# Optimization experiments

Measured on AMD Instinct MI355X. Metric: run time of the kernel, lower is better.

## Reference

```python
import jax, jax.numpy as jnp
import numpy as np
import math

B, T, C, H = 8, 512, 768, 12
ADJ_F = 12  # adj feature dim (adj_proj1 in_features)


def setup_inputs() -> dict:
    key = jax.random.key(0)
    ks = jax.random.split(key, 16)
    s = 0.02
    x = jax.random.normal(ks[0], (B, T, C), jnp.float32)
    # 1.0 marks a padded position; keep first token valid in every row
    pad = (jax.random.uniform(ks[1], (B, T)) > 0.8).astype(jnp.float32)
    pad = pad.at[:, 0].set(0.0)
    adj = jax.random.normal(ks[2], (B, T, T, ADJ_F), jnp.float32)
    # torch Linear convention: W is [out, in]
    Wq = jax.random.normal(ks[3], (C, C), jnp.float32) * s
    bq = jnp.zeros((C,), jnp.float32)
    Wk = jax.random.normal(ks[4], (C, C), jnp.float32) * s
    bk = jnp.zeros((C,), jnp.float32)
    Wv = jax.random.normal(ks[5], (C, C), jnp.float32) * s
    bv = jnp.zeros((C,), jnp.float32)
    Wp = jax.random.normal(ks[6], (C, C), jnp.float32) * s
    bp = jnp.zeros((C,), jnp.float32)
    A1 = jax.random.normal(ks[7], (2 * H, ADJ_F), jnp.float32) * s  # adj_proj1, no bias
    A2 = jax.random.normal(ks[8], (H, 2 * H), jnp.float32) * s     # adj_proj2, no bias
    adj_weight = jnp.float32(50.0)
    return dict(x=x, x_padding_judge=pad, adj=adj, Wq=Wq, bq=bq, Wk=Wk, bk=bk,
                Wv=Wv, bv=bv, Wp=Wp, bp=bp, A1=A1, A2=A2, adj_weight=adj_weight)


def reference(x, x_padding_judge, adj, Wq, bq, Wk, bk, Wv, bv, Wp, bp, A1, A2, adj_weight):
    Bx, Tx, Cx = x.shape
    hd = Cx // H
    # pairwise validity mask: [B,T,T]
    keep = 1.0 - x_padding_judge
    mask = keep[:, :, None] * keep[:, None, :]
    split = lambda h: h.reshape(Bx, Tx, H, hd).transpose(0, 2, 1, 3)  # [B,H,T,hd]
    q = split(x @ Wq.T + bq)
    k = split(x @ Wk.T + bk)
    v = split(x @ Wv.T + bv)
    att = jnp.einsum('bhqd,bhkd->bhqk', q, k) * (1.0 / math.sqrt(hd))
    # eval mode: attn_drop is identity, so the dropout-of-ones trick leaves mask unchanged
    att = jnp.where(mask[:, None, :, :] == 0.0, jnp.float32(-1e9), att)
    att = jax.nn.softmax(att, axis=-1)
    # adjacency-derived bias added AFTER softmax
    att_fix = jax.nn.gelu(jnp.einsum('bqkf,ef->bqke', adj, A1), approximate=False)
    att_fix = jnp.einsum('bqke,he->bqkh', att_fix, A2).transpose(0, 3, 1, 2)  # [B,H,T,T]
    att = att + adj_weight * att_fix
    y = jnp.einsum('bhqk,bhkd->bhqd', att, v)
    y = y.transpose(0, 2, 1, 3).reshape(Bx, Tx, Cx)
    return y @ Wp.T + bp  # resid_drop is identity in eval
```

## Files before the change

kernel.cpp:

```cpp
#include <hip/hip_runtime.h>
#include <math.h>

#define TT 512
#define CC 768
#define NH 12
#define HD 64
#define ADJF 12

typedef __attribute__((ext_vector_type(8))) short bf16x8;
typedef __attribute__((ext_vector_type(4))) float f32x4;

__device__ __forceinline__ ushort f2bf(float x) {
    unsigned u = __float_as_uint(x);
    return (ushort)((u + 0x7FFF + ((u >> 16) & 1)) >> 16);
}

#define MFMA16(a, b, c) __builtin_amdgcn_mfma_f32_16x16x32_bf16((a), (b), (c), 0, 0, 0)

__global__ __launch_bounds__(256)
void cast5(const float* __restrict__ x,  const float* __restrict__ wq,
           const float* __restrict__ wk, const float* __restrict__ wv,
           const float* __restrict__ wp,
           ushort* __restrict__ xb,  ushort* __restrict__ wqb,
           ushort* __restrict__ wkb, ushort* __restrict__ wvb,
           ushort* __restrict__ wpb)
{
    const float* src; ushort* dst; int n8;
    switch (blockIdx.y) {
      case 0:  src = x;  dst = xb;  n8 = 393216; break;
      case 1:  src = wq; dst = wqb; n8 = 73728;  break;
      case 2:  src = wk; dst = wkb; n8 = 73728;  break;
      case 3:  src = wv; dst = wvb; n8 = 73728;  break;
      default: src = wp; dst = wpb; n8 = 73728;  break;
    }
    int i = blockIdx.x * 256 + threadIdx.x;
    if (i >= n8) return;
    float4 a = ((const float4*)src)[2 * i];
    float4 b = ((const float4*)src)[2 * i + 1];
    uint4 o;
    o.x = f2bf(a.x) | ((unsigned)f2bf(a.y) << 16);
    o.y = f2bf(a.z) | ((unsigned)f2bf(a.w) << 16);
    o.z = f2bf(b.x) | ((unsigned)f2bf(b.y) << 16);
    o.w = f2bf(b.z) | ((unsigned)f2bf(b.w) << 16);
    ((uint4*)dst)[i] = o;
}

__device__ __forceinline__ void mfma_gemm_acc(
    const ushort* __restrict__ A, const ushort* __restrict__ B,
    f32x4 (&acc)[4][4], ushort* As, ushort* Bs)
{
    const int t = threadIdx.x;
    const int bm = blockIdx.x, bn = blockIdx.y;
    const int w = t >> 6, lane = t & 63, lx = lane & 15, quad = lane >> 4;
    const int wr = w >> 1, wc = w & 1;
    const int sr = t >> 1, sh = (t & 1) << 4;

    const ushort* Arow = A + (size_t)(bm * 128 + sr) * CC + sh;
    const ushort* Brow = B + (size_t)(bn * 128 + sr) * CC + sh;

    uint4 a0 = *(const uint4*)(Arow);
    uint4 a1 = *(const uint4*)(Arow + 8);
    uint4 b0 = *(const uint4*)(Brow);
    uint4 b1 = *(const uint4*)(Brow + 8);
    *(uint4*)&As[sr * 40 + sh]     = a0;
    *(uint4*)&As[sr * 40 + sh + 8] = a1;
    *(uint4*)&Bs[sr * 40 + sh]     = b0;
    *(uint4*)&Bs[sr * 40 + sh + 8] = b1;

    for (int kb = 0; kb < 24; kb++) {
        __syncthreads();
        const int cur = (kb & 1) * 5120, nxt = ((kb + 1) & 1) * 5120;
        if (kb < 23) {
            a0 = *(const uint4*)(Arow + (kb + 1) * 32);
            a1 = *(const uint4*)(Arow + (kb + 1) * 32 + 8);
            b0 = *(const uint4*)(Brow + (kb + 1) * 32);
            b1 = *(const uint4*)(Brow + (kb + 1) * 32 + 8);
        }
        bf16x8 af[4], bfr[4];
#pragma unroll
        for (int mt = 0; mt < 4; mt++)
            af[mt] = *(const bf16x8*)&As[cur + (wr * 64 + mt * 16 + lx) * 40 + quad * 8];
#pragma unroll
        for (int nt = 0; nt < 4; nt++)
            bfr[nt] = *(const bf16x8*)&Bs[cur + (wc * 64 + nt * 16 + lx) * 40 + quad * 8];
#pragma unroll
        for (int mt = 0; mt < 4; mt++)
#pragma unroll
            for (int nt = 0; nt < 4; nt++)
                acc[mt][nt] = MFMA16(af[mt], bfr[nt], acc[mt][nt]);
        if (kb < 23) {
            *(uint4*)&As[nxt + sr * 40 + sh]     = a0;
            *(uint4*)&As[nxt + sr * 40 + sh + 8] = a1;
            *(uint4*)&Bs[nxt + sr * 40 + sh]     = b0;
            *(uint4*)&Bs[nxt + sr * 40 + sh + 8] = b1;
        }
    }
}

__global__ __launch_bounds__(256)
void qkv_mfma(const ushort* __restrict__ xb,
              const ushort* __restrict__ Wqb, const float* __restrict__ bq,
              const ushort* __restrict__ Wkb, const float* __restrict__ bk,
              const ushort* __restrict__ Wvb, const float* __restrict__ bv,
              ushort* __restrict__ Qb, ushort* __restrict__ Kb,
              ushort* __restrict__ VtB)
{
    __shared__ ushort As[10240], Bs[10240];
    const int z = blockIdx.z;
    const ushort* W   = (z == 0) ? Wqb : (z == 1) ? Wkb : Wvb;
    const float* bias = (z == 0) ? bq  : (z == 1) ? bk  : bv;

    f32x4 acc[4][4];
#pragma unroll
    for (int i = 0; i < 4; i++)
#pragma unroll
        for (int j = 0; j < 4; j++) acc[i][j] = (f32x4){0.f, 0.f, 0.f, 0.f};

    mfma_gemm_acc(xb, W, acc, As, Bs);

    const int t = threadIdx.x;
    const int w = t >> 6, lane = t & 63, lx = lane & 15, quad = lane >> 4;
    const int wr = w >> 1, wc = w & 1;
    const int bm = blockIdx.x, bn = blockIdx.y;

    float bvv[4];
#pragma unroll
    for (int nt = 0; nt < 4; nt++)
        bvv[nt] = bias[bn * 128 + wc * 64 + nt * 16 + lx];

    if (z < 2) {
        ushort* O = (z == 0) ? Qb : Kb;
#pragma unroll
        for (int mt = 0; mt < 4; mt++) {
            int m0 = bm * 128 + wr * 64 + mt * 16 + quad * 4;
#pragma unroll
            for (int nt = 0; nt < 4; nt++) {
                int n = bn * 128 + wc * 64 + nt * 16 + lx;
#pragma unroll
                for (int i = 0; i < 4; i++)
                    O[(size_t)(m0 + i) * CC + n] = f2bf(acc[mt][nt][i] + bvv[nt]);
            }
        }
    } else {
#pragma unroll
        for (int mt = 0; mt < 4; mt++) {
            int m0 = bm * 128 + wr * 64 + mt * 16 + quad * 4;
            int bb = m0 >> 9, k = m0 & 511;
#pragma unroll
            for (int nt = 0; nt < 4; nt++) {
                int n = bn * 128 + wc * 64 + nt * 16 + lx;
                int hh = n >> 6, d = n & 63;
                ushort4 pk;
                pk.x = f2bf(acc[mt][nt][0] + bvv[nt]);
                pk.y = f2bf(acc[mt][nt][1] + bvv[nt]);
                pk.z = f2bf(acc[mt][nt][2] + bvv[nt]);
                pk.w = f2bf(acc[mt][nt][3] + bvv[nt]);
                *(ushort4*)&VtB[(size_t)((bb * NH + hh) * HD + d) * TT + k] = pk;
            }
        }
    }
}

__global__ __launch_bounds__(256)
void proj_mfma(const ushort* __restrict__ y1, const ushort* __restrict__ Wpb,
               const float* __restrict__ bp, float* __restrict__ out)
{
    __shared__ ushort As[10240], Bs[10240];
    f32x4 acc[4][4];
#pragma unroll
    for (int i = 0; i < 4; i++)
#pragma unroll
        for (int j = 0; j < 4; j++) acc[i][j] = (f32x4){0.f, 0.f, 0.f, 0.f};

    mfma_gemm_acc(y1, Wpb, acc, As, Bs);

    const int t = threadIdx.x;
    const int w = t >> 6, lane = t & 63, lx = lane & 15, quad = lane >> 4;
    const int wr = w >> 1, wc = w & 1;
    const int bm = blockIdx.x, bn = blockIdx.y;
#pragma unroll
    for (int nt = 0; nt < 4; nt++) {
        int n = bn * 128 + wc * 64 + nt * 16 + lx;
        float bvv = bp[n];
#pragma unroll
        for (int mt = 0; mt < 4; mt++) {
            int m0 = bm * 128 + wr * 64 + mt * 16 + quad * 4;
#pragma unroll
            for (int i = 0; i < 4; i++)
                out[(size_t)(m0 + i) * CC + n] = acc[mt][nt][i] + bvv;
        }
    }
}

__global__ __launch_bounds__(256)
void adj_f(const float* __restrict__ adj, const float* __restrict__ A1,
           const float* __restrict__ A2, const float* __restrict__ adjw_p,
           ushort* __restrict__ Fb)
{
    __shared__ float A1s[288];
    __shared__ float A2s[288];
    const int t = threadIdx.x;
    for (int i = t; i < 288; i += 256) { A1s[i] = A1[i]; A2s[i] = A2[i]; }
    __syncthreads();

    const float adjw = adjw_p[0];
    const int k = blockIdx.x * 256 + t;
    const int q = blockIdx.y;
    const int b = blockIdx.z;

    float af[12];
    size_t base = (((size_t)b * TT + q) * TT + k) * ADJF;
    *(float4*)&af[0] = *(const float4*)&adj[base + 0];
    *(float4*)&af[4] = *(const float4*)&adj[base + 4];
    *(float4*)&af[8] = *(const float4*)&adj[base + 8];

    float G[24];
#pragma unroll
    for (int e = 0; e < 24; e++) {
        float a2 = 0.f;
#pragma unroll
        for (int f = 0; f < 12; f++) a2 += A1s[e * 12 + f] * af[f];
        float z  = a2 * 0.70710678118654752f;
        float z2 = z * z;
        float er = z * (1.1283791670955126f + z2 * (-0.37612638903183754f +
                   z2 * (0.11283791670955126f + z2 * (-0.02686617064513125f +
                   z2 * (0.00522397762544218f + z2 * (-0.00085483270234508f))))));
        if (__builtin_expect(fabsf(a2) > 1.0f, 0)) er = erff(z);
        G[e] = 0.5f * a2 * (1.0f + er);
    }
#pragma unroll
    for (int hh = 0; hh < 12; hh++) {
        float a2 = 0.f;
#pragma unroll
        for (int e = 0; e < 24; e++) a2 += A2s[hh * 24 + e] * G[e];
        Fb[((size_t)(b * NH + hh) * TT + q) * TT + k] = f2bf(adjw * a2);
    }
}

__global__ __launch_bounds__(256)
void flash_mfma(const ushort* __restrict__ Qb, const ushort* __restrict__ Kb,
                const ushort* __restrict__ VtB, const ushort* __restrict__ Fb,
                const float* __restrict__ pad, ushort* __restrict__ y1)
{
    __shared__ ushort Ps[4][16][72];

    const int t = threadIdx.x, w = t >> 6, lane = t & 63;
    const int lx = lane & 15, quad = lane >> 4;
    const int qt = blockIdx.x, h = blockIdx.y, b = blockIdx.z;
    const int q0 = qt * 64;
    const int bh = b * NH + h;

    const ushort* Qrow = Qb + (size_t)(b * TT + q0 + w * 16 + lx) * CC + h * HD + quad * 8;
    bf16x8 qa0 = *(const bf16x8*)Qrow;
    bf16x8 qa1 = *(const bf16x8*)(Qrow + 32);

    const float kq = 1.0f - pad[b * TT + q0 + w * 16 + lx];

    f32x4 o[4], o2[4];
#pragma unroll
    for (int i = 0; i < 4; i++) {
        o[i]  = (f32x4){0.f, 0.f, 0.f, 0.f};
        o2[i] = (f32x4){0.f, 0.f, 0.f, 0.f};
    }
    float ls = 0.f;

    const ushort* Frow = Fb + (size_t)(bh * TT + q0 + w * 16 + lx) * TT + quad * 8;
    const float*  padk = pad + b * TT;
    const ushort* Vbase = VtB + (size_t)bh * HD * TT;

    for (int ck = 0; ck < 8; ck++) {
        const int k0 = ck * 64;
        f32x4 st[4];
        float4 kp[4];
#pragma unroll
        for (int mt = 0; mt < 4; mt++) {
            const ushort* Krow = Kb + (size_t)(b * TT + k0 + mt * 16 + lx) * CC + h * HD + quad * 8;
            bf16x8 ka0 = *(const bf16x8*)Krow;
            bf16x8 ka1 = *(const bf16x8*)(Krow + 32);
            f32x4 z = (f32x4){0.f, 0.f, 0.f, 0.f};
            z = MFMA16(ka0, qa0, z);
            z = MFMA16(ka1, qa1, z);
            st[mt] = z;
            kp[mt] = *(const float4*)&padk[k0 + mt * 16 + quad * 4];
        }
#pragma unroll
        for (int mt = 0; mt < 4; mt++) {
            float pv[4];
#pragma unroll
            for (int i = 0; i < 4; i++) {
                float kpad = ((const float*)&kp[mt])[i];
                float p = __builtin_amdgcn_exp2f(st[mt][i] * 0.18033688011112042f);
                p = (kpad != 0.0f) ? 0.0f : p;
                p = (kq == 0.0f) ? 1.0f : p;
                pv[i] = p; ls += p;
            }
            ushort4 pk;
            pk.x = f2bf(pv[0]); pk.y = f2bf(pv[1]);
            pk.z = f2bf(pv[2]); pk.w = f2bf(pv[3]);
            *(ushort4*)&Ps[w][lx][mt * 16 + quad * 4] = pk;
        }
        asm volatile("s_waitcnt lgkmcnt(0)" ::: "memory");
        bf16x8 pa0 = *(const bf16x8*)&Ps[w][lx][quad * 8];
        bf16x8 pa1 = *(const bf16x8*)&Ps[w][lx][32 + quad * 8];
        bf16x8 fa0 = *(const bf16x8*)(Frow + k0);
        bf16x8 fa1 = *(const bf16x8*)(Frow + k0 + 32);
#pragma unroll
        for (int nt = 0; nt < 4; nt++) {
            const ushort* Vrow = Vbase + (size_t)(nt * 16 + lx) * TT + k0 + quad * 8;
            bf16x8 vb0 = *(const bf16x8*)Vrow;
            bf16x8 vb1 = *(const bf16x8*)(Vrow + 32);
            o[nt]  = MFMA16(pa0, vb0, o[nt]);
            o[nt]  = MFMA16(pa1, vb1, o[nt]);
            o2[nt] = MFMA16(fa0, vb0, o2[nt]);
            o2[nt] = MFMA16(fa1, vb1, o2[nt]);
        }
    }
    ls += __shfl_xor(ls, 16, 64);
    ls += __shfl_xor(ls, 32, 64);
    float inv[4];
#pragma unroll
    for (int i = 0; i < 4; i++)
        inv[i] = 1.0f / __shfl(ls, quad * 4 + i, 16);
#pragma unroll
    for (int nt = 0; nt < 4; nt++)
#pragma unroll
        for (int i = 0; i < 4; i++)
            y1[(size_t)(b * TT + q0 + w * 16 + quad * 4 + i) * CC + h * HD + nt * 16 + lx] =
                f2bf(o[nt][i] * inv[i] + o2[nt][i]);
}

extern "C" void kernel_launch(void* const* d_in, const int* in_sizes, int n_in,
                              void* d_out, int out_size, void* d_ws, size_t ws_size,
                              hipStream_t stream)
{
    const float* x    = (const float*)d_in[0];
    const float* pad  = (const float*)d_in[1];
    const float* adj  = (const float*)d_in[2];
    const float* Wq   = (const float*)d_in[3];
    const float* bq   = (const float*)d_in[4];
    const float* Wk   = (const float*)d_in[5];
    const float* bk   = (const float*)d_in[6];
    const float* Wv   = (const float*)d_in[7];
    const float* bv   = (const float*)d_in[8];
    const float* Wp   = (const float*)d_in[9];
    const float* bp   = (const float*)d_in[10];
    const float* A1   = (const float*)d_in[11];
    const float* A2   = (const float*)d_in[12];
    const float* adjw = (const float*)d_in[13];

    ushort* ws  = (ushort*)d_ws;
    ushort* Fb  = ws;
    ushort* Qb  = Fb + 25165824;
    ushort* Kb  = Qb + 3145728;
    ushort* Vt  = Kb + 3145728;
    ushort* y1  = Vt + 3145728;
    ushort* xb  = y1 + 3145728;
    ushort* Wqb = xb + 3145728;
    ushort* Wkb = Wqb + 589824;
    ushort* Wvb = Wkb + 589824;
    ushort* Wpb = Wvb + 589824;
    float*  out = (float*)d_out;

    cast5<<<dim3(1536, 5), 256, 0, stream>>>(x, Wq, Wk, Wv, Wp,
                                             xb, Wqb, Wkb, Wvb, Wpb);
    qkv_mfma<<<dim3(32, 6, 3), 256, 0, stream>>>(xb, Wqb, bq, Wkb, bk, Wvb, bv,
                                                 Qb, Kb, Vt);
    adj_f<<<dim3(2, 512, 8), 256, 0, stream>>>(adj, A1, A2, adjw, Fb);
    flash_mfma<<<dim3(8, 12, 8), 256, 0, stream>>>(Qb, Kb, Vt, Fb, pad, y1);
    proj_mfma<<<dim3(32, 6), 256, 0, stream>>>(y1, Wpb, bp, out);
}
```

Baseline: 314.3 us.

## Compute adjacency bias projections with bf16 MFMA instead of scalar FMAs

The adjacency kernel now does the two small projections (12->24 and 24->12) as bf16 16x16x32 MFMAs. The GELU intermediates are staged through per-wave LDS, and the erf polynomial is shortened, with its exact-erf fallback threshold lowered. The aim is to cut the VALU-bound scalar FMA and polynomial work in the adj_f stage, which reads the large adj tensor. In exchange it adds bf16 rounding of the adj inputs and weights, wastes MFMA lanes because K is padded, and makes 16-lane partial float4 loads.

```diff
diff --git a/kernel.cpp b/kernel.cpp
--- a/kernel.cpp
+++ b/kernel.cpp
@@ -192,48 +192,82 @@
     }
 }
 
+__device__ __forceinline__ float gelu_s(float x) {
+    float z  = x * 0.70710678118654752f;
+    float z2 = z * z;
+    float er = z * (1.1283791670955126f + z2 * (-0.37612638903183754f +
+               z2 * 0.11283791670955126f));
+    if (__builtin_expect(fabsf(x) > 0.5f, 0)) er = erff(z);
+    return 0.5f * x * (1.0f + er);
+}
+
 __global__ __launch_bounds__(256)
-void adj_f(const float* __restrict__ adj, const float* __restrict__ A1,
-           const float* __restrict__ A2, const float* __restrict__ adjw_p,
-           ushort* __restrict__ Fb)
+void adj_f_mfma(const float* __restrict__ adj, const float* __restrict__ A1,
+                const float* __restrict__ A2, const float* __restrict__ adjw_p,
+                ushort* __restrict__ Fb)
 {
     __shared__ float A1s[288];
     __shared__ float A2s[288];
+    __shared__ ushort Gs[4][2][16][40];
+
     const int t = threadIdx.x;
     for (int i = t; i < 288; i += 256) { A1s[i] = A1[i]; A2s[i] = A2[i]; }
     __syncthreads();
 
+    const int w = t >> 6, lane = t & 63, lx = lane & 15, qd = lane >> 4;
+    const int q = blockIdx.x, b = blockIdx.y;
     const float adjw = adjw_p[0];
-    const int k = blockIdx.x * 256 + t;
-    const int q = blockIdx.y;
-    const int b = blockIdx.z;
-
-    float af[12];
-    size_t base = (((size_t)b * TT + q) * TT + k) * ADJF;
-    *(float4*)&af[0] = *(const float4*)&adj[base + 0];
-    *(float4*)&af[4] = *(const float4*)&adj[base + 4];
-    *(float4*)&af[8] = *(const float4*)&adj[base + 8];
-
-    float G[24];
-#pragma unroll
-    for (int e = 0; e < 24; e++) {
-        float a2 = 0.f;
-#pragma unroll
-        for (int f = 0; f < 12; f++) a2 += A1s[e * 12 + f] * af[f];
-        float z  = a2 * 0.70710678118654752f;
-        float z2 = z * z;
-        float er = z * (1.1283791670955126f + z2 * (-0.37612638903183754f +
-                   z2 * (0.11283791670955126f + z2 * (-0.02686617064513125f +
-                   z2 * (0.00522397762544218f + z2 * (-0.00085483270234508f))))));
-        if (__builtin_expect(fabsf(a2) > 1.0f, 0)) er = erff(z);
-        G[e] = 0.5f * a2 * (1.0f + er);
-    }
-#pragma unroll
-    for (int hh = 0; hh < 12; hh++) {
-        float a2 = 0.f;
-#pragma unroll
-        for (int e = 0; e < 24; e++) a2 += A2s[hh * 24 + e] * G[e];
-        Fb[((size_t)(b * NH + hh) * TT + q) * TT + k] = f2bf(adjw * a2);
+
+    union { bf16x8 v; ushort u[8]; } b1a, b1b, b2;
+#pragma unroll
+    for (int j = 0; j < 8; j++) {
+        int f = qd * 8 + j;
+        b1a.u[j] = (f < 12) ? f2bf(A1s[lx * 12 + f]) : 0;
+        b1b.u[j] = (lx < 8 && f < 12) ? f2bf(A1s[(16 + lx) * 12 + f]) : 0;
+        b2.u[j]  = (lx < 12 && f < 24) ? f2bf(adjw * A2s[lx * 24 + f]) : 0;
+    }
+
+    const size_t prow = ((size_t)b * TT + q) * TT;
+    ushort* outq = Fb + ((size_t)(b * NH) * TT + q) * TT;
+
+    for (int it = 0; it < 8; it++) {
+        const int k0 = it * 64 + w * 16;
+        const int p  = it & 1;
+        union { bf16x8 v; ushort u[8]; } afr;
+        const float* arow = adj + (prow + k0 + lx) * ADJF;
+        if (qd == 0) {
+            float4 u0 = *(const float4*)(arow);
+            float4 u1 = *(const float4*)(arow + 4);
+            afr.u[0] = f2bf(u0.x); afr.u[1] = f2bf(u0.y);
+            afr.u[2] = f2bf(u0.z); afr.u[3] = f2bf(u0.w);
+            afr.u[4] = f2bf(u1.x); afr.u[5] = f2bf(u1.y);
+            afr.u[6] = f2bf(u1.z); afr.u[7] = f2bf(u1.w);
+        } else if (qd == 1) {
+            float4 u0 = *(const float4*)(arow + 8);
+            afr.u[0] = f2bf(u0.x); afr.u[1] = f2bf(u0.y);
+            afr.u[2] = f2bf(u0.z); afr.u[3] = f2bf(u0.w);
+            afr.u[4] = 0; afr.u[5] = 0; afr.u[6] = 0; afr.u[7] = 0;
+        } else {
+#pragma unroll
+            for (int j = 0; j < 8; j++) afr.u[j] = 0;
+        }
+        f32x4 zz = (f32x4){0.f, 0.f, 0.f, 0.f};
+        f32x4 c1a = MFMA16(afr.v, b1a.v, zz);
+        f32x4 c1b = MFMA16(afr.v, b1b.v, zz);
+#pragma unroll
+        for (int i = 0; i < 4; i++) {
+            Gs[w][p][qd * 4 + i][lx]      = f2bf(gelu_s(c1a[i]));
+            Gs[w][p][qd * 4 + i][16 + lx] = f2bf(gelu_s(c1b[i]));
+        }
+        asm volatile("s_waitcnt lgkmcnt(0)" ::: "memory");
+        bf16x8 a2f = *(const bf16x8*)&Gs[w][p][lx][qd * 8];
+        f32x4 c2 = MFMA16(a2f, b2.v, zz);
+        if (lx < 12) {
+            ushort4 pk;
+            pk.x = f2bf(c2[0]); pk.y = f2bf(c2[1]);
+            pk.z = f2bf(c2[2]); pk.w = f2bf(c2[3]);
+            *(ushort4*)&outq[(size_t)lx * TT * TT + k0 + qd * 4] = pk;
+        }
     }
 }
 
@@ -365,7 +399,7 @@
                                              xb, Wqb, Wkb, Wvb, Wpb);
     qkv_mfma<<<dim3(32, 6, 3), 256, 0, stream>>>(xb, Wqb, bq, Wkb, bk, Wvb, bv,
                                                  Qb, Kb, Vt);
-    adj_f<<<dim3(2, 512, 8), 256, 0, stream>>>(adj, A1, A2, adjw, Fb);
+    adj_f_mfma<<<dim3(512, 8), 256, 0, stream>>>(adj, A1, A2, adjw, Fb);
     flash_mfma<<<dim3(8, 12, 8), 256, 0, stream>>>(Qb, Kb, Vt, Fb, pad, y1);
     proj_mfma<<<dim3(32, 6), 256, 0, stream>>>(y1, Wpb, bp, out);
 }
```

Result: no change. 310.4 us (-1.2%).
